# Performance work log

Hardware: AMD Instinct MI355X
Metric: run time of the kernel (lower is better)

Reference implementation:

```python
import jax, jax.numpy as jnp
import numpy as np

N = 200000      # total nodes
NG = 100000     # masked (graph) nodes
NU = N - NG     # unconnected nodes
E = 3200000     # edges (index into graph nodes)
C = 1000000     # candidate pairs


def setup_inputs() -> dict:
    key = jax.random.key(0)
    ks = jax.random.split(key, 16)
    s = 0.1  # weight init scale
    x = jax.random.normal(ks[0], (N, 2), jnp.float32)
    mask = jnp.arange(N) < NG
    candidates = jnp.stack([
        jax.random.randint(ks[1], (C,), 0, NG),
        jax.random.randint(ks[2], (C,), 0, NU),
    ], axis=1).astype(jnp.int32)
    edges = jax.random.randint(ks[3], (2, E), 0, NG).astype(jnp.int32)
    return {
        "x": x, "mask": mask, "candidates": candidates, "edges": edges,
        # GraphConv(2,8): lin_rel on aggregated neighbors, lin_root on self, bias in rel
        "w1_rel": jax.random.normal(ks[4], (2, 8), jnp.float32) * s,
        "w1_root": jax.random.normal(ks[5], (2, 8), jnp.float32) * s,
        "b1": jnp.zeros((8,), jnp.float32),
        # GraphConv(8,16)
        "w2_rel": jax.random.normal(ks[6], (8, 16), jnp.float32) * s,
        "w2_root": jax.random.normal(ks[7], (8, 16), jnp.float32) * s,
        "b2": jnp.zeros((16,), jnp.float32),
        # fc_unconnected: Linear(2,16) (source's Linear(8,16) is inconsistent with 2-dim x)
        "wu": jax.random.normal(ks[8], (2, 16), jnp.float32) * s,
        "bu": jnp.zeros((16,), jnp.float32),
        # fc: Linear(32,64) -> ReLU -> Linear(64,1)
        "wa": jax.random.normal(ks[9], (32, 64), jnp.float32) * s,
        "ba": jnp.zeros((64,), jnp.float32),
        "wb": jax.random.normal(ks[10], (64, 1), jnp.float32) * s,
        "bb": jnp.zeros((1,), jnp.float32),
    }


def graph_conv(h, edges, w_rel, w_root, b, n):
    # PyG GraphConv with aggr='add': out_i = W_rel @ sum_{j->i} h_j + W_root @ h_i + b
    src, dst = edges[0], edges[1]
    agg = jax.ops.segment_sum(h[src], dst, num_segments=n)  # [n, d_in]
    return agg @ w_rel + h @ w_root + b


def reference(x, mask, candidates, edges, w1_rel, w1_root, b1,
              w2_rel, w2_root, b2, wu, bu, wa, ba, wb, bb):
    idx_g = jnp.nonzero(mask, size=NG)[0]      # graph node indices
    idx_u = jnp.nonzero(~mask, size=NU)[0]     # unconnected node indices
    x_unconnected = x[idx_u] @ wu + bu                         # [NU, 16]
    h = jax.nn.relu(graph_conv(x[idx_g], edges, w1_rel, w1_root, b1, NG))  # [NG, 8]
    h = jax.nn.relu(graph_conv(h, edges, w2_rel, w2_root, b2, NG))         # [NG, 16]
    ec = jnp.concatenate([h[candidates[:, 0]], x_unconnected[candidates[:, 1]]], axis=-1)  # [C, 32]
    hid = jax.nn.relu(ec @ wa + ba)            # [C, 64]
    return jnp.squeeze(hid @ wb + bb, -1)      # [C]
```

## Files before the change

kernel.cpp:

```cpp
#include <hip/hip_runtime.h>

#define N_TOT  200000
#define NG_    100000
#define NU_    100000
#define E_CNT  3200000
#define C_CNT  1000000

#define NBUCK  196
#define NBLK   256
#define CHUNK  12500

__global__ __launch_bounds__(256) void phaseA(const int* __restrict__ dst,
                                              int* __restrict__ cnt_mat) {
    __shared__ int hcnt[NBUCK];
    int t = threadIdx.x;
    if (t < NBUCK) hcnt[t] = 0;
    __syncthreads();
    int beg = blockIdx.x * CHUNK, end = beg + CHUNK;
    for (int e = beg + t; e < end; e += 256)
        atomicAdd(&hcnt[dst[e] >> 9], 1);
    __syncthreads();
    if (t < NBUCK) cnt_mat[blockIdx.x * NBUCK + t] = hcnt[t];
}

__global__ __launch_bounds__(256) void phaseB1(const int* __restrict__ cnt_mat,
                                               int* __restrict__ off_mat,
                                               int* __restrict__ colsum) {
    __shared__ int s[256];
    int t = threadIdx.x;
    int k = blockIdx.x;
    int v = cnt_mat[t * NBUCK + k];
    s[t] = v;
    __syncthreads();
    for (int off = 1; off < 256; off <<= 1) {
        int u = (t >= off) ? s[t - off] : 0;
        __syncthreads();
        s[t] += u;
        __syncthreads();
    }
    off_mat[t * NBUCK + k] = s[t] - v;
    if (t == 255) colsum[k] = s[255];
}

__global__ __launch_bounds__(256) void phaseB2(const int* __restrict__ colsum,
                                               int* __restrict__ bbase) {
    __shared__ int s[256];
    int t = threadIdx.x;
    int v = (t < NBUCK) ? colsum[t] : 0;
    s[t] = v;
    __syncthreads();
    for (int off = 1; off < 256; off <<= 1) {
        int u = (t >= off) ? s[t - off] : 0;
        __syncthreads();
        s[t] += u;
        __syncthreads();
    }
    if (t < NBUCK) bbase[t] = s[t] - v;
    if (t == NBUCK - 1) bbase[NBUCK] = s[t];
}

__global__ __launch_bounds__(256) void phaseC(const int* __restrict__ src,
                                              const int* __restrict__ dst,
                                              const int* __restrict__ off_mat,
                                              const int* __restrict__ bbase,
                                              int* __restrict__ pairs) {
    __shared__ int loc[NBUCK];
    int t = threadIdx.x;
    if (t < NBUCK) loc[t] = bbase[t] + off_mat[blockIdx.x * NBUCK + t];
    __syncthreads();
    int beg = blockIdx.x * CHUNK, end = beg + CHUNK;
    for (int e = beg + t; e < end; e += 256) {
        int d = dst[e], s = src[e];
        int k = d >> 9;
        int pos = atomicAdd(&loc[k], 1);
        pairs[pos] = (s << 9) | (d & 511);
    }
}

__global__ __launch_bounds__(1024) void phaseD(const int* __restrict__ bbase,
                                               const int* __restrict__ pairs,
                                               int* __restrict__ csr_src,
                                               int* __restrict__ node_off) {
    __shared__ int cnt[512], scn[512], base[512];
    int t = threadIdx.x, k = blockIdx.x;
    if (t < 512) cnt[t] = 0;
    __syncthreads();
    int beg = bbase[k], end = bbase[k + 1];
    for (int e = beg + t; e < end; e += 1024)
        atomicAdd(&cnt[pairs[e] & 511], 1);
    __syncthreads();
    if (t < 512) scn[t] = cnt[t];
    __syncthreads();
    for (int off = 1; off < 512; off <<= 1) {
        int v = 0;
        if (t < 512 && t >= off) v = scn[t - off];
        __syncthreads();
        if (t < 512) scn[t] += v;
        __syncthreads();
    }
    if (t < 512) {
        int bse = beg + scn[t] - cnt[t];
        base[t] = bse;
        node_off[(k << 9) + t] = bse;
    }
    __syncthreads();
    for (int e = beg + t; e < end; e += 1024) {
        int p = pairs[e];
        int pos = atomicAdd(&base[p & 511], 1);
        csr_src[pos] = p >> 9;
    }
}

__global__ __launch_bounds__(256) void conv1_csr(const int* __restrict__ node_off,
                                                 const int* __restrict__ csr_src,
                                                 const float* __restrict__ x,
                                                 const float* __restrict__ w_rel,
                                                 const float* __restrict__ w_root,
                                                 const float* __restrict__ b,
                                                 float* __restrict__ h1) {
    int t = threadIdx.x;
    int n = blockIdx.x * 32 + (t >> 3);
    int l = t & 7;
    int beg = node_off[n], end = node_off[n + 1];
    float a0 = 0.f, a1 = 0.f;
    for (int e = beg + l; e < end; e += 8) {
        int s = csr_src[e];
        float2 xv = *(const float2*)(x + 2 * s);
        a0 += xv.x; a1 += xv.y;
    }
#pragma unroll
    for (int d = 1; d < 8; d <<= 1) {
        a0 += __shfl_xor(a0, d, 64);
        a1 += __shfl_xor(a1, d, 64);
    }
    float2 xn = *(const float2*)(x + 2 * n);
    float v = a0 * w_rel[l] + a1 * w_rel[8 + l]
            + xn.x * w_root[l] + xn.y * w_root[8 + l] + b[l];
    h1[8 * n + l] = fmaxf(v, 0.f);
}

__global__ __launch_bounds__(256) void conv2_csr(const int* __restrict__ node_off,
                                                 const int* __restrict__ csr_src,
                                                 const float* __restrict__ h1,
                                                 const float* __restrict__ w_rel,
                                                 const float* __restrict__ w_root,
                                                 const float* __restrict__ b,
                                                 float* __restrict__ h2) {
    int t = threadIdx.x;
    int n = blockIdx.x * 32 + (t >> 3);
    int l = t & 7;
    int beg = node_off[n], end = node_off[n + 1];
    float acc[8] = {0.f, 0.f, 0.f, 0.f, 0.f, 0.f, 0.f, 0.f};
    for (int e = beg + l; e < end; e += 8) {
        int s = csr_src[e];
        const float4* hp = (const float4*)(h1 + 8 * s);
        float4 v0 = hp[0], v1 = hp[1];
        acc[0] += v0.x; acc[1] += v0.y; acc[2] += v0.z; acc[3] += v0.w;
        acc[4] += v1.x; acc[5] += v1.y; acc[6] += v1.z; acc[7] += v1.w;
    }
#pragma unroll
    for (int d = 1; d < 8; d <<= 1)
#pragma unroll
        for (int j = 0; j < 8; j++)
            acc[j] += __shfl_xor(acc[j], d, 64);
    const float4* hp = (const float4*)(h1 + 8 * n);
    float4 t0 = hp[0], t1 = hp[1];
    float hn[8] = {t0.x, t0.y, t0.z, t0.w, t1.x, t1.y, t1.z, t1.w};
#pragma unroll
    for (int cc = 0; cc < 2; cc++) {
        int c = l + 8 * cc;
        float v = b[c];
#pragma unroll
        for (int j = 0; j < 8; j++)
            v += acc[j] * w_rel[j * 16 + c] + hn[j] * w_root[j * 16 + c];
        h2[16 * n + c] = fmaxf(v, 0.f);
    }
}

__global__ void prep_kernel(const float* __restrict__ wu,
                            const float* __restrict__ bu,
                            const float* __restrict__ wa,
                            const float* __restrict__ ba,
                            float* __restrict__ wprep) {
    int j = threadIdx.x;
#pragma unroll
    for (int i = 0; i < 16; i++) wprep[j * 16 + i] = wa[i * 64 + j];
    float c0 = 0.f, c1 = 0.f, bc = ba[j];
#pragma unroll
    for (int k = 0; k < 16; k++) {
        float w = wa[(16 + k) * 64 + j];
        c0 += wu[k] * w;
        c1 += wu[16 + k] * w;
        bc += bu[k] * w;
    }
    wprep[1024 + j] = c0;
    wprep[1088 + j] = c1;
    wprep[1152 + j] = bc;
}

__global__ __launch_bounds__(256) void precompA(const float* __restrict__ h2,
                                                const float* __restrict__ wa,
                                                const float* __restrict__ wprep,
                                                float* __restrict__ Ag) {
    int g = blockIdx.x * 256 + threadIdx.x;
    if (g >= NG_) return;
    float h[16];
    const float4* hp = (const float4*)(h2 + 16 * g);
#pragma unroll
    for (int q = 0; q < 4; q++) {
        float4 v = hp[q];
        h[4*q] = v.x; h[4*q+1] = v.y; h[4*q+2] = v.z; h[4*q+3] = v.w;
    }
    float4* op = (float4*)(Ag + 64 * g);
#pragma unroll
    for (int q = 0; q < 16; q++) {
        float4 v;
        v.x = wprep[1152 + 4*q + 0];
        v.y = wprep[1152 + 4*q + 1];
        v.z = wprep[1152 + 4*q + 2];
        v.w = wprep[1152 + 4*q + 3];
#pragma unroll
        for (int i = 0; i < 16; i++) {
            float hi = h[i];
            v.x += hi * wa[i*64 + 4*q + 0];
            v.y += hi * wa[i*64 + 4*q + 1];
            v.z += hi * wa[i*64 + 4*q + 2];
            v.w += hi * wa[i*64 + 4*q + 3];
        }
        op[q] = v;
    }
}

__global__ __launch_bounds__(256) void final_mlp3(const int* __restrict__ cand,
                                                  const float* __restrict__ Ag,
                                                  const float* __restrict__ x,
                                                  const float* __restrict__ wprep,
                                                  const float* __restrict__ wb,
                                                  const float* __restrict__ bb,
                                                  float* __restrict__ out) {
    int c = blockIdx.x * 256 + threadIdx.x;
    if (c >= C_CNT) return;
    int g = cand[2 * c], u = cand[2 * c + 1];
    float2 xv = *(const float2*)(x + 2 * (NG_ + u));
    const float4* ap = (const float4*)(Ag + 64 * g);
    float acc = bb[0];
#pragma unroll
    for (int q = 0; q < 16; q++) {
        float4 a = ap[q];
        float v0 = a.x + xv.x * wprep[1024 + 4*q + 0] + xv.y * wprep[1088 + 4*q + 0];
        float v1 = a.y + xv.x * wprep[1024 + 4*q + 1] + xv.y * wprep[1088 + 4*q + 1];
        float v2 = a.z + xv.x * wprep[1024 + 4*q + 2] + xv.y * wprep[1088 + 4*q + 2];
        float v3 = a.w + xv.x * wprep[1024 + 4*q + 3] + xv.y * wprep[1088 + 4*q + 3];
        acc += fmaxf(v0, 0.f) * wb[4*q + 0];
        acc += fmaxf(v1, 0.f) * wb[4*q + 1];
        acc += fmaxf(v2, 0.f) * wb[4*q + 2];
        acc += fmaxf(v3, 0.f) * wb[4*q + 3];
    }
    out[c] = acc;
}


extern "C" void kernel_launch(void* const* d_in, const int* in_sizes, int n_in,
                              void* d_out, int out_size, void* d_ws, size_t ws_size,
                              hipStream_t stream) {
    const float* x      = (const float*)d_in[0];
    const int*   cand   = (const int*)d_in[2];
    const int*   edges  = (const int*)d_in[3];
    const float* w1_rel = (const float*)d_in[4];
    const float* w1_root= (const float*)d_in[5];
    const float* b1     = (const float*)d_in[6];
    const float* w2_rel = (const float*)d_in[7];
    const float* w2_root= (const float*)d_in[8];
    const float* b2     = (const float*)d_in[9];
    const float* wu     = (const float*)d_in[10];
    const float* bu     = (const float*)d_in[11];
    const float* wa     = (const float*)d_in[12];
    const float* ba     = (const float*)d_in[13];
    const float* wb     = (const float*)d_in[14];
    const float* bb     = (const float*)d_in[15];
    float* out = (float*)d_out;

    const int* src = edges;
    const int* dst = edges + E_CNT;

    int* ws_i = (int*)d_ws;
    int*   cnt_mat  = ws_i;
    int*   off_mat  = ws_i + 50176;
    int*   colsum   = ws_i + 100352;
    int*   bbase    = ws_i + 100608;
    int*   node_off = ws_i + 100864;
    float* wprep    = (float*)(ws_i + 201728);
    int*   pairs    = ws_i + 202944;
    int*   csr_src  = ws_i + 3402944;
    float* h1       = (float*)(ws_i + 6602944);
    float* h2       = (float*)(ws_i + 7402944);
    float* Ag       = (float*)(ws_i + 202944);

    dim3 blk256(256);

    prep_kernel<<<1, 64, 0, stream>>>(wu, bu, wa, ba, wprep);
    phaseA <<<NBLK, blk256, 0, stream>>>(dst, cnt_mat);
    phaseB1<<<NBUCK, blk256, 0, stream>>>(cnt_mat, off_mat, colsum);
    phaseB2<<<1, blk256, 0, stream>>>(colsum, bbase);
    phaseC <<<NBLK, blk256, 0, stream>>>(src, dst, off_mat, bbase, pairs);
    phaseD <<<NBUCK, 1024, 0, stream>>>(bbase, pairs, csr_src, node_off);
    conv1_csr<<<3125, blk256, 0, stream>>>(node_off, csr_src, x, w1_rel, w1_root, b1, h1);
    conv2_csr<<<3125, blk256, 0, stream>>>(node_off, csr_src, h1, w2_rel, w2_root, b2, h2);
    precompA<<<(NG_ + 255) / 256, blk256, 0, stream>>>(h2, wa, wprep, Ag);
    final_mlp3<<<(C_CNT + 255) / 256, blk256, 0, stream>>>(cand, Ag, x, wprep, wb, bb, out);
}
```

Baseline: 275.1 us.

## Bucket-sort candidates by graph node before final MLP for gather locality

Measured after the change: 302.0 us. 1.1x slower.

```diff
diff --git a/kernel.cpp b/kernel.cpp
--- a/kernel.cpp
+++ b/kernel.cpp
@@ -9,6 +9,9 @@
 #define NBUCK  196
 #define NBLK   256
 #define CHUNK  12500
+
+#define CBLK   250
+#define CCHUNK 4000
 
 __global__ __launch_bounds__(256) void phaseA(const int* __restrict__ dst,
                                               int* __restrict__ cnt_mat) {
@@ -231,7 +234,75 @@
     }
 }
 
-__global__ __launch_bounds__(256) void final_mlp3(const int* __restrict__ cand,
+__global__ __launch_bounds__(256) void candA(const int* __restrict__ cand,
+                                             int* __restrict__ cnt2) {
+    __shared__ int hcnt[NBUCK];
+    int t = threadIdx.x;
+    if (t < NBUCK) hcnt[t] = 0;
+    __syncthreads();
+    int beg = blockIdx.x * CCHUNK, end = beg + CCHUNK;
+    for (int e = beg + t; e < end; e += 256)
+        atomicAdd(&hcnt[cand[2 * e] >> 9], 1);
+    __syncthreads();
+    if (t < NBUCK) cnt2[blockIdx.x * NBUCK + t] = hcnt[t];
+}
+
+__global__ __launch_bounds__(256) void candB1(const int* __restrict__ cnt2,
+                                              int* __restrict__ off2,
+                                              int* __restrict__ csum2) {
+    __shared__ int s[256];
+    int t = threadIdx.x;
+    int k = blockIdx.x;
+    int v = (t < CBLK) ? cnt2[t * NBUCK + k] : 0;
+    s[t] = v;
+    __syncthreads();
+    for (int off = 1; off < 256; off <<= 1) {
+        int u = (t >= off) ? s[t - off] : 0;
+        __syncthreads();
+        s[t] += u;
+        __syncthreads();
+    }
+    if (t < CBLK) off2[t * NBUCK + k] = s[t] - v;
+    if (t == 255) csum2[k] = s[255];
+}
+
+__global__ __launch_bounds__(256) void candB2(const int* __restrict__ csum2,
+                                              int* __restrict__ bbase2) {
+    __shared__ int s[256];
+    int t = threadIdx.x;
+    int v = (t < NBUCK) ? csum2[t] : 0;
+    s[t] = v;
+    __syncthreads();
+    for (int off = 1; off < 256; off <<= 1) {
+        int u = (t >= off) ? s[t - off] : 0;
+        __syncthreads();
+        s[t] += u;
+        __syncthreads();
+    }
+    if (t < NBUCK) bbase2[t] = s[t] - v;
+    if (t == NBUCK - 1) bbase2[NBUCK] = s[t];
+}
+
+__global__ __launch_bounds__(256) void candC(const int* __restrict__ cand,
+                                             const int* __restrict__ off2,
+                                             const int* __restrict__ bbase2,
+                                             int2* __restrict__ sc) {
+    __shared__ int loc[NBUCK];
+    int t = threadIdx.x;
+    if (t < NBUCK) loc[t] = bbase2[t] + off2[blockIdx.x * NBUCK + t];
+    __syncthreads();
+    int beg = blockIdx.x * CCHUNK, end = beg + CCHUNK;
+    for (int e = beg + t; e < end; e += 256) {
+        int g = cand[2 * e], u = cand[2 * e + 1];
+        int k = g >> 9;
+        int pos = atomicAdd(&loc[k], 1);
+        int w0 = g | (u << 17);
+        int w1 = (int)(((unsigned)u >> 15) | ((unsigned)e << 2));
+        sc[pos] = make_int2(w0, w1);
+    }
+}
+
+__global__ __launch_bounds__(256) void final_mlp4(const int2* __restrict__ sc,
                                                   const float* __restrict__ Ag,
                                                   const float* __restrict__ x,
                                                   const float* __restrict__ wprep,
@@ -240,7 +311,11 @@
                                                   float* __restrict__ out) {
     int c = blockIdx.x * 256 + threadIdx.x;
     if (c >= C_CNT) return;
-    int g = cand[2 * c], u = cand[2 * c + 1];
+    int2 w = sc[c];
+    unsigned w0 = (unsigned)w.x, w1 = (unsigned)w.y;
+    int g   = (int)(w0 & 0x1FFFFu);
+    int u   = (int)((w0 >> 17) | ((w1 & 3u) << 15));
+    int idx = (int)(w1 >> 2);
     float2 xv = *(const float2*)(x + 2 * (NG_ + u));
     const float4* ap = (const float4*)(Ag + 64 * g);
     float acc = bb[0];
@@ -256,7 +331,7 @@
         acc += fmaxf(v2, 0.f) * wb[4*q + 2];
         acc += fmaxf(v3, 0.f) * wb[4*q + 3];
     }
-    out[c] = acc;
+    out[idx] = acc;
 }
 
 
@@ -295,6 +370,11 @@
     float* h1       = (float*)(ws_i + 6602944);
     float* h2       = (float*)(ws_i + 7402944);
     float* Ag       = (float*)(ws_i + 202944);
+    int*   cnt2     = ws_i;
+    int*   off2     = ws_i + 50176;
+    int*   csum2    = ws_i + 100352;
+    int*   bbase2   = ws_i + 100608;
+    int2*  sc       = (int2*)(ws_i + 6602944);
 
     dim3 blk256(256);
 
@@ -307,5 +387,9 @@
     conv1_csr<<<3125, blk256, 0, stream>>>(node_off, csr_src, x, w1_rel, w1_root, b1, h1);
     conv2_csr<<<3125, blk256, 0, stream>>>(node_off, csr_src, h1, w2_rel, w2_root, b2, h2);
     precompA<<<(NG_ + 255) / 256, blk256, 0, stream>>>(h2, wa, wprep, Ag);
-    final_mlp3<<<(C_CNT + 255) / 256, blk256, 0, stream>>>(cand, Ag, x, wprep, wb, bb, out);
-}
+    candA <<<CBLK, blk256, 0, stream>>>(cand, cnt2);
+    candB1<<<NBUCK, blk256, 0, stream>>>(cnt2, off2, csum2);
+    candB2<<<1, blk256, 0, stream>>>(csum2, bbase2);
+    candC <<<CBLK, blk256, 0, stream>>>(cand, off2, bbase2, sc);
+    final_mlp4<<<(C_CNT + 255) / 256, blk256, 0, stream>>>(sc, Ag, x, wprep, wb, bb, out);
+}
```
